# Kernel tuning notes

Hardware: AMD Instinct MI355X
Metric: run time of the kernel (lower is better)

Reference implementation:

```python
import jax, jax.numpy as jnp
import numpy as np

B, S, D, H = 4, 2048, 1024, 16
HD = D // H
SCALE = D ** (-0.5)  # NOTE: original scales by embedding_dim**-0.5, not head_size**-0.5


def setup_inputs() -> dict:
    key = jax.random.key(0)
    k1, k2, k3, k4, k5 = jax.random.split(key, 5)
    return {
        "x": jax.random.normal(k1, (B, S, D), dtype=jnp.float32),
        "Wqkv": jax.random.normal(k2, (3 * D, D), dtype=jnp.float32) * (D ** -0.5),
        "bqkv": jax.random.normal(k3, (3 * D,), dtype=jnp.float32) * 0.02,
        "Wlift": jax.random.normal(k4, (D, D), dtype=jnp.float32) * (D ** -0.5),
        "blift": jax.random.normal(k5, (D,), dtype=jnp.float32) * 0.02,
    }


def reference(x, Wqkv, bqkv, Wlift, blift):
    b, s, d = x.shape
    # qkv projection -> (b, s, 3, H, HD) -> (3, b, H, s, HD)
    qkv = (x @ Wqkv.T + bqkv).reshape(b, s, 3, H, HD).transpose(2, 0, 3, 1, 4)
    q, k, v = qkv[0], qkv[1], qkv[2]  # each (b, H, s, HD)
    # full score matrix, softmax over keys
    scores = jnp.einsum("bhqd,bhkd->bhqk", q, k) * SCALE
    a = jax.nn.softmax(scores, axis=-1)
    # post-hoc causal mask + renormalize (as in the original)
    a = jnp.tril(a)
    a = a / jnp.sum(a, axis=-1, keepdims=True)
    attn = jnp.einsum("bhqk,bhkd->bhqd", a, v)  # (b, H, s, HD)
    attn = attn.swapaxes(1, 2).reshape(b, s, d)  # (b, s, d)
    # lifting linear; Dropout(0.2) is identity in eval mode
    return attn @ Wlift.T + blift
```

## Files before the change

### kernel.cpp

```cpp
#include <hip/hip_runtime.h>
#include <cstdint>
#include <cstddef>

typedef unsigned short u16;
typedef unsigned int u32;
typedef __bf16 bf16x8 __attribute__((ext_vector_type(8)));
typedef float f32x4 __attribute__((ext_vector_type(4)));
typedef float f32x16 __attribute__((ext_vector_type(16)));

__device__ __forceinline__ u16 f2bf(float f) {
  unsigned u = __builtin_bit_cast(unsigned, f);
  return (u16)((u + 0x7FFFu + ((u >> 16) & 1u)) >> 16);
}

__device__ __forceinline__ u32 pk2bf(float lo, float hi) {
  union { __bf16 h[2]; u32 u; } t;
  t.h[0] = (__bf16)lo; t.h[1] = (__bf16)hi;
  return t.u;
}

__device__ __forceinline__ void gl_lds16(const void* g, void* l) {
  __builtin_amdgcn_global_load_lds(
      (const __attribute__((address_space(1))) unsigned int*)g,
      (__attribute__((address_space(3))) unsigned int*)l,
      16, 0, 0);
}

__global__ void cast_all_kernel(const float* __restrict__ x, u16* __restrict__ xo,
                                const float* __restrict__ wq, u16* __restrict__ wqo,
                                const float* __restrict__ wl, u16* __restrict__ wlo) {
  int i = blockIdx.x * blockDim.x + threadIdx.x;
  const float* src;
  u16* dst;
  int k;
  if (i < 2097152) { src = x; dst = xo; k = i; }
  else if (i < 2883584) { src = wq; dst = wqo; k = i - 2097152; }
  else { src = wl; dst = wlo; k = i - 2883584; }
  float4 v = reinterpret_cast<const float4*>(src)[k];
  ushort4 o;
  o.x = f2bf(v.x); o.y = f2bf(v.y); o.z = f2bf(v.z); o.w = f2bf(v.w);
  reinterpret_cast<ushort4*>(dst)[k] = o;
}

template <int EPI>
__global__ __launch_bounds__(256)
void gemm_bt_kernel(const u16* __restrict__ A, const u16* __restrict__ Bw,
                    const float* __restrict__ bias,
                    u16* __restrict__ oq, u16* __restrict__ ok, u16* __restrict__ ovT,
                    float* __restrict__ ofp, int M, int N, int K) {
  __shared__ __align__(16) u16 Als[2][128 * 32];
  __shared__ __align__(16) u16 Bls[2][128 * 32];

  const int tid = threadIdx.x;
  const int lane = tid & 63;
  const int w = tid >> 6, wr = w >> 1, wc = w & 1;
  const int lr = lane & 15, lk = lane >> 4;

  const int nbx = N >> 7;
  const int nb = (M >> 7) * nbx;
  const int vb = (blockIdx.x & 7) * (nb >> 3) + (blockIdx.x >> 3);
  const int brow = (vb / nbx) * 128, bcol = (vb % nbx) * 128;

  const int srow = tid >> 2;
  const int scol = (tid & 3) << 3;
  const u16* ga = A + (size_t)(brow + srow) * K + scol;
  const u16* gb = Bw + (size_t)(bcol + srow) * K + scol;

  f32x4 acc[4][4] = {};

  auto stage = [&](int buf, int kt) {
    const u16* a0 = ga + kt * 32;
    const u16* b0 = gb + kt * 32;
    gl_lds16(a0,             &Als[buf][tid * 8]);
    gl_lds16(a0 + 64 * K,    &Als[buf][2048 + tid * 8]);
    gl_lds16(b0,             &Bls[buf][tid * 8]);
    gl_lds16(b0 + 64 * K,    &Bls[buf][2048 + tid * 8]);
  };

  stage(0, 0);
  __syncthreads();

  const int nt = K >> 5;
  int cur = 0;
  for (int t = 0; t < nt; ++t) {
    if (t + 1 < nt) stage(cur ^ 1, t + 1);
    bf16x8 af[4], bfr[4];
#pragma unroll
    for (int m = 0; m < 4; ++m)
      af[m] = *reinterpret_cast<const bf16x8*>(&Als[cur][(wr * 64 + m * 16 + lr) * 32 + lk * 8]);
#pragma unroll
    for (int n = 0; n < 4; ++n)
      bfr[n] = *reinterpret_cast<const bf16x8*>(&Bls[cur][(wc * 64 + n * 16 + lr) * 32 + lk * 8]);
#pragma unroll
    for (int m = 0; m < 4; ++m)
#pragma unroll
      for (int n = 0; n < 4; ++n)
        acc[m][n] = __builtin_amdgcn_mfma_f32_16x16x32_bf16(af[m], bfr[n], acc[m][n], 0, 0, 0);
    __syncthreads();
    cur ^= 1;
  }

  if (EPI == 0) {
    const int three = bcol >> 10;
#pragma unroll
    for (int n = 0; n < 4; ++n) {
      const int c = bcol + wc * 64 + n * 16 + lr;
      const float bv = bias[c];
      const int cc = c & 1023, h = cc >> 6, hd = cc & 63;
#pragma unroll
      for (int m = 0; m < 4; ++m) {
        const int r0 = brow + wr * 64 + m * 16 + lk * 4;
        const int b = r0 >> 11;
        const int s0 = r0 & 2047;
        if (three == 2) {
          ushort4 pkv;
          pkv.x = f2bf(acc[m][n][0] + bv);
          pkv.y = f2bf(acc[m][n][1] + bv);
          pkv.z = f2bf(acc[m][n][2] + bv);
          pkv.w = f2bf(acc[m][n][3] + bv);
          *reinterpret_cast<ushort4*>(&ovT[((size_t)(b * 16 + h) * 64 + hd) * 2048 + s0]) = pkv;
        } else {
          u16* dst = (three == 0) ? oq : ok;
          const float sc = (three == 0) ? 0.03125f * 1.44269504089f : 1.0f;
#pragma unroll
          for (int j = 0; j < 4; ++j)
            dst[((size_t)(b * 16 + h) * 2048 + (s0 + j)) * 64 + hd] = f2bf((acc[m][n][j] + bv) * sc);
        }
      }
    }
  } else {
#pragma unroll
    for (int n = 0; n < 4; ++n) {
      const int c = bcol + wc * 64 + n * 16 + lr;
      const float bv = bias[c];
#pragma unroll
      for (int m = 0; m < 4; ++m) {
        const int r0 = brow + wr * 64 + m * 16 + lk * 4;
#pragma unroll
        for (int j = 0; j < 4; ++j)
          ofp[(size_t)(r0 + j) * N + c] = acc[m][n][j] + bv;
      }
    }
  }
}

__global__ __launch_bounds__(256, 3)
void attn_causal_kernel(const u16* __restrict__ qg, const u16* __restrict__ kg_,
                        const u16* __restrict__ vT, u16* __restrict__ ob) {
  __shared__ __align__(16) u16 Kls[3][64 * 64];
  __shared__ __align__(16) u16 Vls[3][64 * 64];

  const int tid = threadIdx.x, lane = tid & 63, w = tid >> 6;
  const int n = lane & 31, hi = lane >> 5;
  const int bid = blockIdx.x;
  const int qbi = 15 - (bid >> 6);
  const int bh = bid & 63;
  const int q0w = qbi * 128 + w * 32;
  const int jdiag = qbi * 4 + w;
  const size_t base = (size_t)bh * 2048 * 64;
  const size_t vbase = (size_t)bh * 64 * 2048;

  bf16x8 qf[4];
#pragma unroll
  for (int dc = 0; dc < 4; ++dc)
    qf[dc] = *reinterpret_cast<const bf16x8*>(
        &qg[base + (size_t)(q0w + n) * 64 + dc * 16 + hi * 8]);

  f32x16 o0 = {}, o1 = {};
  float l = 0.f;

  const int ktiles = qbi * 2 + 2;

  const int krow = tid >> 3, kch = tid & 7;

  auto stage = [&](int buf, int t) {
    const int k0 = t << 6;
#pragma unroll
    for (int p = 0; p < 2; ++p) {
      const int r = p * 32 + krow;
      const int sz = (r ^ (r >> 3)) & 7;
      gl_lds16(kg_ + base + (size_t)(k0 + r) * 64 + (kch ^ sz) * 8,
               &Kls[buf][p * 2048 + tid * 8]);
      gl_lds16(vT + vbase + (size_t)r * 2048 + k0 + (kch ^ sz) * 8,
               &Vls[buf][p * 2048 + tid * 8]);
    }
  };

  const int sw0 = ((n ^ (n >> 3)) & 7) << 4;
  const int sw1 = (((32 + n) ^ ((32 + n) >> 3)) & 7) << 4;

  stage(0, 0);
  stage(1, ktiles > 1 ? 1 : 0);
  asm volatile("s_waitcnt vmcnt(4)" ::: "memory");
  __builtin_amdgcn_sched_barrier(0);
  __builtin_amdgcn_s_barrier();
  __builtin_amdgcn_sched_barrier(0);

  bf16x8 pbP0 = {}, pbP1 = {}, vfP00 = {}, vfP01 = {}, vfP10 = {}, vfP11 = {};
  bool pend = false;

  union U { u32 u[4]; bf16x8 v; };

  auto slab = [&](const char* Kb, const char* Vb, int mt, bool diag) {
    const int swK = mt ? sw1 : sw0;
    f32x16 st = {};
    __builtin_amdgcn_s_setprio(1);
#pragma unroll
    for (int dc = 0; dc < 4; ++dc) {
      bf16x8 kf = *reinterpret_cast<const bf16x8*>(
          Kb + (mt * 32 + n) * 128 + ((((dc << 1) | hi) << 4) ^ swK));
      st = __builtin_amdgcn_mfma_f32_32x32x16_bf16(kf, qf[dc], st, 0, 0, 0);
    }
    if (pend) {
      o0 = __builtin_amdgcn_mfma_f32_32x32x16_bf16(vfP00, pbP0, o0, 0, 0, 0);
      o1 = __builtin_amdgcn_mfma_f32_32x32x16_bf16(vfP01, pbP0, o1, 0, 0, 0);
      o0 = __builtin_amdgcn_mfma_f32_32x32x16_bf16(vfP10, pbP1, o0, 0, 0, 0);
      o1 = __builtin_amdgcn_mfma_f32_32x32x16_bf16(vfP11, pbP1, o1, 0, 0, 0);
    }
    __builtin_amdgcn_s_setprio(0);
    if (diag) {
#pragma unroll
      for (int r = 0; r < 16; ++r) {
        const int koff = (r & 3) + 8 * (r >> 2) + 4 * hi;
        if (koff > n) st[r] = -1e30f;
      }
    }
    float rs = 0.f;
#pragma unroll
    for (int r = 0; r < 16; ++r) { st[r] = __builtin_amdgcn_exp2f(st[r]); rs += st[r]; }
    l += rs;
#pragma unroll
    for (int kk = 0; kk < 2; ++kk) {
      const int gown = (kk * 2 + hi) * 4, gsnd = (kk * 2 + (hi ^ 1)) * 4;
      u32 pa0 = pk2bf(st[gown + 0], st[gown + 1]);
      u32 pa1 = pk2bf(st[gown + 2], st[gown + 3]);
      u32 ps0 = pk2bf(st[gsnd + 0], st[gsnd + 1]);
      u32 ps1 = pk2bf(st[gsnd + 2], st[gsnd + 3]);
      u32 rA = __shfl_xor(ps0, 32, 64);
      u32 rB = __shfl_xor(ps1, 32, 64);
      U pb;
      pb.u[0] = hi ? rA : pa0;
      pb.u[1] = hi ? rB : pa1;
      pb.u[2] = hi ? pa0 : rA;
      pb.u[3] = hi ? pa1 : rB;
      if (kk == 0) pbP0 = pb.v; else pbP1 = pb.v;
    }
    const int c0 = ((mt * 4 + hi) << 4);
    const int c1 = ((mt * 4 + 2 + hi) << 4);
    vfP00 = *reinterpret_cast<const bf16x8*>(Vb + n * 128 + (c0 ^ sw0));
    vfP01 = *reinterpret_cast<const bf16x8*>(Vb + (32 + n) * 128 + (c0 ^ sw1));
    vfP10 = *reinterpret_cast<const bf16x8*>(Vb + n * 128 + (c1 ^ sw0));
    vfP11 = *reinterpret_cast<const bf16x8*>(Vb + (32 + n) * 128 + (c1 ^ sw1));
    pend = true;
  };

  for (int t = 0; t < ktiles; ++t) {
    const int tpre = (t + 2 < ktiles) ? (t + 2) : (ktiles - 1);
    stage((t + 2) % 3, tpre);
    const char* Kb = (const char*)&Kls[t % 3][0];
    const char* Vb = (const char*)&Vls[t % 3][0];
    const int e0 = 2 * t;
    if (e0 <= jdiag) slab(Kb, Vb, 0, e0 == jdiag);
    if (e0 + 1 <= jdiag) slab(Kb, Vb, 1, e0 + 1 == jdiag);
    asm volatile("s_waitcnt vmcnt(4)" ::: "memory");
    __builtin_amdgcn_sched_barrier(0);
    __builtin_amdgcn_s_barrier();
    __builtin_amdgcn_sched_barrier(0);
  }

  if (pend) {
    __builtin_amdgcn_s_setprio(1);
    o0 = __builtin_amdgcn_mfma_f32_32x32x16_bf16(vfP00, pbP0, o0, 0, 0, 0);
    o1 = __builtin_amdgcn_mfma_f32_32x32x16_bf16(vfP01, pbP0, o1, 0, 0, 0);
    o0 = __builtin_amdgcn_mfma_f32_32x32x16_bf16(vfP10, pbP1, o0, 0, 0, 0);
    o1 = __builtin_amdgcn_mfma_f32_32x32x16_bf16(vfP11, pbP1, o1, 0, 0, 0);
    __builtin_amdgcn_s_setprio(0);
  }

  asm volatile("s_waitcnt vmcnt(0)" ::: "memory");

  const int b = bh >> 4, h = bh & 15;
  const float lt = l + __shfl_xor(l, 32, 64);
  const float inv = 1.f / lt;
  const size_t rbase = ((size_t)(b * 2048 + q0w + n)) * 1024 + h * 64;
#pragma unroll
  for (int g = 0; g < 4; ++g) {
    ushort4 w0, w1;
    w0.x = f2bf(o0[g * 4 + 0] * inv); w0.y = f2bf(o0[g * 4 + 1] * inv);
    w0.z = f2bf(o0[g * 4 + 2] * inv); w0.w = f2bf(o0[g * 4 + 3] * inv);
    w1.x = f2bf(o1[g * 4 + 0] * inv); w1.y = f2bf(o1[g * 4 + 1] * inv);
    w1.z = f2bf(o1[g * 4 + 2] * inv); w1.w = f2bf(o1[g * 4 + 3] * inv);
    *reinterpret_cast<ushort4*>(&ob[rbase + g * 8 + hi * 4]) = w0;
    *reinterpret_cast<ushort4*>(&ob[rbase + 32 + g * 8 + hi * 4]) = w1;
  }
}

extern "C" void kernel_launch(void* const* d_in, const int* in_sizes, int n_in,
                              void* d_out, int out_size, void* d_ws, size_t ws_size,
                              hipStream_t stream) {
  const float* x     = (const float*)d_in[0];
  const float* Wqkv  = (const float*)d_in[1];
  const float* bqkv  = (const float*)d_in[2];
  const float* Wlift = (const float*)d_in[3];
  const float* blift = (const float*)d_in[4];
  float* out = (float*)d_out;

  if (ws_size < 40ull * 1024 * 1024) return;

  char* ws = (char*)d_ws;
  u16* xb     = (u16*)(ws);
  u16* wqkvb  = (u16*)(ws + 16777216);
  u16* wliftb = (u16*)(ws + 23068672);
  u16* vT     = (u16*)(ws + 25165824);
  u16* attnb  = xb;
  u16* qb = (u16*)d_out;
  u16* kb = qb + 8388608;

  cast_all_kernel<<<12288, 256, 0, stream>>>(x, xb, Wqkv, wqkvb, Wlift, wliftb);

  gemm_bt_kernel<0><<<1536, 256, 0, stream>>>(
      xb, wqkvb, bqkv, qb, kb, vT, nullptr, 8192, 3072, 1024);

  attn_causal_kernel<<<1024, 256, 0, stream>>>(qb, kb, vT, attnb);

  gemm_bt_kernel<1><<<512, 256, 0, stream>>>(
      attnb, wliftb, blift, nullptr, nullptr, nullptr, out, 8192, 1024, 1024);
}
```

Measured before the change: 259.7 us.

## Add dedicated 256x256-tile QKV GEMM with swizzled LDS and wider K step

```diff
diff --git a/kernel.cpp b/kernel.cpp
--- a/kernel.cpp
+++ b/kernel.cpp
@@ -42,12 +42,136 @@
   reinterpret_cast<ushort4*>(dst)[k] = o;
 }
 
-template <int EPI>
+__global__ __launch_bounds__(512, 2)
+void gemm256_qkv_kernel(const u16* __restrict__ A, const u16* __restrict__ Bw,
+                        const float* __restrict__ bias,
+                        u16* __restrict__ oq, u16* __restrict__ ok,
+                        u16* __restrict__ ovT) {
+  __shared__ __align__(16) u16 Als[2][256 * 64];
+  __shared__ __align__(16) u16 Bls[2][256 * 64];
+
+  const int tid = threadIdx.x, lane = tid & 63;
+  const int w = tid >> 6, wr = w >> 2, wc = w & 3;
+  const int lr = lane & 15, lk = lane >> 4;
+
+  const int local = blockIdx.x >> 3, x = blockIdx.x & 7;
+  const int bcol = (local >> 2) * 256;
+  const int brow = (x * 4 + (local & 3)) * 256;
+
+  const u16* ga[4];
+  const u16* gb[4];
+  int dsl[4];
+#pragma unroll
+  for (int p = 0; p < 4; ++p) {
+    const int s = tid + p * 512;
+    const int row = s >> 3, ch = s & 7;
+    const int sc = ch ^ (row & 7);
+    ga[p] = A + (size_t)(brow + row) * 1024 + sc * 8;
+    gb[p] = Bw + (size_t)(bcol + row) * 1024 + sc * 8;
+    dsl[p] = s * 8;
+  }
+
+  auto stage = [&](int buf, int kt) {
+#pragma unroll
+    for (int p = 0; p < 4; ++p) {
+      gl_lds16(ga[p] + kt * 64, &Als[buf][dsl[p]]);
+      gl_lds16(gb[p] + kt * 64, &Bls[buf][dsl[p]]);
+    }
+  };
+
+  f32x4 acc[2][2][4][2] = {};
+
+  stage(0, 0);
+  asm volatile("s_waitcnt vmcnt(0)" ::: "memory");
+  __builtin_amdgcn_s_barrier();
+  __builtin_amdgcn_sched_barrier(0);
+
+  for (int t = 0; t < 16; ++t) {
+    const int buf = t & 1;
+    const char* Ab = (const char*)&Als[buf][0];
+    const char* Bb = (const char*)&Bls[buf][0];
+    if (t + 1 < 16) stage(buf ^ 1, t + 1);
+#pragma unroll
+    for (int mq = 0; mq < 2; ++mq)
+#pragma unroll
+      for (int nq = 0; nq < 2; ++nq) {
+        bf16x8 af[4][2], bfr[2][2];
+#pragma unroll
+        for (int m = 0; m < 4; ++m) {
+          const int ar = wr * 128 + mq * 64 + m * 16 + lr;
+          const int asw = (ar & 7) << 4;
+#pragma unroll
+          for (int ks = 0; ks < 2; ++ks)
+            af[m][ks] = *reinterpret_cast<const bf16x8*>(
+                Ab + ar * 128 + ((ks * 64 + lk * 16) ^ asw));
+        }
+#pragma unroll
+        for (int n = 0; n < 2; ++n) {
+          const int br = wc * 64 + nq * 32 + n * 16 + lr;
+          const int bsw = (br & 7) << 4;
+#pragma unroll
+          for (int ks = 0; ks < 2; ++ks)
+            bfr[n][ks] = *reinterpret_cast<const bf16x8*>(
+                Bb + br * 128 + ((ks * 64 + lk * 16) ^ bsw));
+        }
+        asm volatile("s_waitcnt lgkmcnt(0)" ::: "memory");
+        __builtin_amdgcn_sched_barrier(0);
+        __builtin_amdgcn_s_setprio(1);
+#pragma unroll
+        for (int ks = 0; ks < 2; ++ks)
+#pragma unroll
+          for (int m = 0; m < 4; ++m)
+#pragma unroll
+            for (int n = 0; n < 2; ++n)
+              acc[mq][nq][m][n] = __builtin_amdgcn_mfma_f32_16x16x32_bf16(
+                  af[m][ks], bfr[n][ks], acc[mq][nq][m][n], 0, 0, 0);
+        __builtin_amdgcn_s_setprio(0);
+      }
+    asm volatile("s_waitcnt vmcnt(0)" ::: "memory");
+    __builtin_amdgcn_s_barrier();
+    __builtin_amdgcn_sched_barrier(0);
+  }
+
+  const int three = bcol >> 10;
+#pragma unroll
+  for (int mq = 0; mq < 2; ++mq)
+#pragma unroll
+    for (int nq = 0; nq < 2; ++nq)
+#pragma unroll
+      for (int n = 0; n < 2; ++n) {
+        const int c = bcol + wc * 64 + nq * 32 + n * 16 + lr;
+        const float bv = bias[c];
+        const int cc = c & 1023, h = cc >> 6, hd = cc & 63;
+#pragma unroll
+        for (int m = 0; m < 4; ++m) {
+          const int r0 = brow + wr * 128 + mq * 64 + m * 16 + lk * 4;
+          const int b = r0 >> 11;
+          const int s0 = r0 & 2047;
+          const f32x4& a4 = acc[mq][nq][m][n];
+          if (three == 2) {
+            ushort4 pkv;
+            pkv.x = f2bf(a4[0] + bv);
+            pkv.y = f2bf(a4[1] + bv);
+            pkv.z = f2bf(a4[2] + bv);
+            pkv.w = f2bf(a4[3] + bv);
+            *reinterpret_cast<ushort4*>(
+                &ovT[((size_t)(b * 16 + h) * 64 + hd) * 2048 + s0]) = pkv;
+          } else {
+            u16* dst = (three == 0) ? oq : ok;
+            const float sc = (three == 0) ? 0.03125f * 1.44269504089f : 1.0f;
+#pragma unroll
+            for (int j = 0; j < 4; ++j)
+              dst[((size_t)(b * 16 + h) * 2048 + (s0 + j)) * 64 + hd] =
+                  f2bf((a4[j] + bv) * sc);
+          }
+        }
+      }
+}
+
 __global__ __launch_bounds__(256)
-void gemm_bt_kernel(const u16* __restrict__ A, const u16* __restrict__ Bw,
-                    const float* __restrict__ bias,
-                    u16* __restrict__ oq, u16* __restrict__ ok, u16* __restrict__ ovT,
-                    float* __restrict__ ofp, int M, int N, int K) {
+void gemm_lift_kernel(const u16* __restrict__ A, const u16* __restrict__ Bw,
+                      const float* __restrict__ bias, float* __restrict__ ofp,
+                      int M, int N, int K) {
   __shared__ __align__(16) u16 Als[2][128 * 32];
   __shared__ __align__(16) u16 Bls[2][128 * 32];
 
@@ -100,46 +224,16 @@
     cur ^= 1;
   }
 
-  if (EPI == 0) {
-    const int three = bcol >> 10;
-#pragma unroll
-    for (int n = 0; n < 4; ++n) {
-      const int c = bcol + wc * 64 + n * 16 + lr;
-      const float bv = bias[c];
-      const int cc = c & 1023, h = cc >> 6, hd = cc & 63;
-#pragma unroll
-      for (int m = 0; m < 4; ++m) {
-        const int r0 = brow + wr * 64 + m * 16 + lk * 4;
-        const int b = r0 >> 11;
-        const int s0 = r0 & 2047;
-        if (three == 2) {
-          ushort4 pkv;
-          pkv.x = f2bf(acc[m][n][0] + bv);
-          pkv.y = f2bf(acc[m][n][1] + bv);
-          pkv.z = f2bf(acc[m][n][2] + bv);
-          pkv.w = f2bf(acc[m][n][3] + bv);
-          *reinterpret_cast<ushort4*>(&ovT[((size_t)(b * 16 + h) * 64 + hd) * 2048 + s0]) = pkv;
-        } else {
-          u16* dst = (three == 0) ? oq : ok;
-          const float sc = (three == 0) ? 0.03125f * 1.44269504089f : 1.0f;
-#pragma unroll
-          for (int j = 0; j < 4; ++j)
-            dst[((size_t)(b * 16 + h) * 2048 + (s0 + j)) * 64 + hd] = f2bf((acc[m][n][j] + bv) * sc);
-        }
-      }
-    }
-  } else {
-#pragma unroll
-    for (int n = 0; n < 4; ++n) {
-      const int c = bcol + wc * 64 + n * 16 + lr;
-      const float bv = bias[c];
-#pragma unroll
-      for (int m = 0; m < 4; ++m) {
-        const int r0 = brow + wr * 64 + m * 16 + lk * 4;
-#pragma unroll
-        for (int j = 0; j < 4; ++j)
-          ofp[(size_t)(r0 + j) * N + c] = acc[m][n][j] + bv;
-      }
+#pragma unroll
+  for (int n = 0; n < 4; ++n) {
+    const int c = bcol + wc * 64 + n * 16 + lr;
+    const float bv = bias[c];
+#pragma unroll
+    for (int m = 0; m < 4; ++m) {
+      const int r0 = brow + wr * 64 + m * 16 + lk * 4;
+#pragma unroll
+      for (int j = 0; j < 4; ++j)
+        ofp[(size_t)(r0 + j) * N + c] = acc[m][n][j] + bv;
     }
   }
 }
@@ -318,11 +412,10 @@
 
   cast_all_kernel<<<12288, 256, 0, stream>>>(x, xb, Wqkv, wqkvb, Wlift, wliftb);
 
-  gemm_bt_kernel<0><<<1536, 256, 0, stream>>>(
-      xb, wqkvb, bqkv, qb, kb, vT, nullptr, 8192, 3072, 1024);
+  gemm256_qkv_kernel<<<384, 512, 0, stream>>>(xb, wqkvb, bqkv, qb, kb, vT);
 
   attn_causal_kernel<<<1024, 256, 0, stream>>>(qb, kb, vT, attnb);
 
-  gemm_bt_kernel<1><<<512, 256, 0, stream>>>(
-      attnb, wliftb, blift, nullptr, nullptr, nullptr, out, 8192, 1024, 1024);
-}
+  gemm_lift_kernel<<<512, 256, 0, stream>>>(
+      attnb, wliftb, blift, out, 8192, 1024, 1024);
+}
```

Measured after the change: 273.7 us. 5.4% more time.

## Split causal attention KV range across two blocks with atomic fp32 combine

Applied to the files above, without the earlier changes.

```diff
diff --git a/kernel.cpp b/kernel.cpp
--- a/kernel.cpp
+++ b/kernel.cpp
@@ -144,19 +144,24 @@
   }
 }
 
-__global__ __launch_bounds__(256, 3)
-void attn_causal_kernel(const u16* __restrict__ qg, const u16* __restrict__ kg_,
-                        const u16* __restrict__ vT, u16* __restrict__ ob) {
-  __shared__ __align__(16) u16 Kls[3][64 * 64];
-  __shared__ __align__(16) u16 Vls[3][64 * 64];
+__global__ __launch_bounds__(256, 5)
+void attn_split_kernel(const u16* __restrict__ qg, const u16* __restrict__ kg_,
+                       const u16* __restrict__ vT, float* __restrict__ Of,
+                       float* __restrict__ lf) {
+  __shared__ __align__(16) u16 Kls[2][64 * 64];
+  __shared__ __align__(16) u16 Vls[2][64 * 64];
 
   const int tid = threadIdx.x, lane = tid & 63, w = tid >> 6;
   const int n = lane & 31, hi = lane >> 5;
   const int bid = blockIdx.x;
-  const int qbi = 15 - (bid >> 6);
-  const int bh = bid & 63;
+  const int half = bid & 1;
+  const int rest = bid >> 1;
+  const int qbi = 15 - (rest >> 6);
+  const int bh = rest & 63;
   const int q0w = qbi * 128 + w * 32;
   const int jdiag = qbi * 4 + w;
+  const int t0 = half ? (qbi + 1) : 0;
+  const int ntiles = qbi + 1;
   const size_t base = (size_t)bh * 2048 * 64;
   const size_t vbase = (size_t)bh * 64 * 2048;
 
@@ -168,8 +173,6 @@
 
   f32x16 o0 = {}, o1 = {};
   float l = 0.f;
-
-  const int ktiles = qbi * 2 + 2;
 
   const int krow = tid >> 3, kch = tid & 7;
 
@@ -189,12 +192,8 @@
   const int sw0 = ((n ^ (n >> 3)) & 7) << 4;
   const int sw1 = (((32 + n) ^ ((32 + n) >> 3)) & 7) << 4;
 
-  stage(0, 0);
-  stage(1, ktiles > 1 ? 1 : 0);
-  asm volatile("s_waitcnt vmcnt(4)" ::: "memory");
-  __builtin_amdgcn_sched_barrier(0);
-  __builtin_amdgcn_s_barrier();
-  __builtin_amdgcn_sched_barrier(0);
+  stage(0, t0);
+  __syncthreads();
 
   bf16x8 pbP0 = {}, pbP1 = {}, vfP00 = {}, vfP01 = {}, vfP10 = {}, vfP11 = {};
   bool pend = false;
@@ -254,6 +253,163 @@
     pend = true;
   };
 
+  for (int tt = 0; tt < ntiles; ++tt) {
+    const int t = t0 + tt;
+    if (tt + 1 < ntiles) stage((tt + 1) & 1, t + 1);
+    const char* Kb = (const char*)&Kls[tt & 1][0];
+    const char* Vb = (const char*)&Vls[tt & 1][0];
+    const int e0 = 2 * t;
+    if (e0 <= jdiag) slab(Kb, Vb, 0, e0 == jdiag);
+    if (e0 + 1 <= jdiag) slab(Kb, Vb, 1, e0 + 1 == jdiag);
+    __syncthreads();
+  }
+
+  if (pend) {
+    __builtin_amdgcn_s_setprio(1);
+    o0 = __builtin_amdgcn_mfma_f32_32x32x16_bf16(vfP00, pbP0, o0, 0, 0, 0);
+    o1 = __builtin_amdgcn_mfma_f32_32x32x16_bf16(vfP01, pbP0, o1, 0, 0, 0);
+    o0 = __builtin_amdgcn_mfma_f32_32x32x16_bf16(vfP10, pbP1, o0, 0, 0, 0);
+    o1 = __builtin_amdgcn_mfma_f32_32x32x16_bf16(vfP11, pbP1, o1, 0, 0, 0);
+    __builtin_amdgcn_s_setprio(0);
+  }
+
+  const float lt = l + __shfl_xor(l, 32, 64);
+  const size_t qrow = (size_t)bh * 2048 + q0w + n;
+  if (hi == 0) atomicAdd(&lf[qrow], lt);
+  float* Orow = Of + qrow * 64;
+#pragma unroll
+  for (int r = 0; r < 16; ++r) {
+    const int d = (r & 3) + 8 * (r >> 2) + 4 * hi;
+    atomicAdd(&Orow[d], o0[r]);
+    atomicAdd(&Orow[32 + d], o1[r]);
+  }
+}
+
+__global__ __launch_bounds__(256)
+void combine_kernel(const float* __restrict__ Of, const float* __restrict__ lf,
+                    u16* __restrict__ ob) {
+  const int tid = blockIdx.x * 256 + threadIdx.x;
+  const int row = tid >> 4;
+  const int d4 = (tid & 15) * 4;
+  const int bh = row >> 11, q = row & 2047;
+  const int b = bh >> 4, h = bh & 15;
+  const float inv = 1.f / lf[row];
+  const float4 v = *reinterpret_cast<const float4*>(Of + (size_t)row * 64 + d4);
+  ushort4 o;
+  o.x = f2bf(v.x * inv); o.y = f2bf(v.y * inv);
+  o.z = f2bf(v.z * inv); o.w = f2bf(v.w * inv);
+  *reinterpret_cast<ushort4*>(&ob[((size_t)(b * 2048 + q)) * 1024 + h * 64 + d4]) = o;
+}
+
+__global__ __launch_bounds__(256, 3)
+void attn_causal_kernel(const u16* __restrict__ qg, const u16* __restrict__ kg_,
+                        const u16* __restrict__ vT, u16* __restrict__ ob) {
+  __shared__ __align__(16) u16 Kls[3][64 * 64];
+  __shared__ __align__(16) u16 Vls[3][64 * 64];
+
+  const int tid = threadIdx.x, lane = tid & 63, w = tid >> 6;
+  const int n = lane & 31, hi = lane >> 5;
+  const int bid = blockIdx.x;
+  const int qbi = 15 - (bid >> 6);
+  const int bh = bid & 63;
+  const int q0w = qbi * 128 + w * 32;
+  const int jdiag = qbi * 4 + w;
+  const size_t base = (size_t)bh * 2048 * 64;
+  const size_t vbase = (size_t)bh * 64 * 2048;
+
+  bf16x8 qf[4];
+#pragma unroll
+  for (int dc = 0; dc < 4; ++dc)
+    qf[dc] = *reinterpret_cast<const bf16x8*>(
+        &qg[base + (size_t)(q0w + n) * 64 + dc * 16 + hi * 8]);
+
+  f32x16 o0 = {}, o1 = {};
+  float l = 0.f;
+
+  const int ktiles = qbi * 2 + 2;
+  const int krow = tid >> 3, kch = tid & 7;
+
+  auto stage = [&](int buf, int t) {
+    const int k0 = t << 6;
+#pragma unroll
+    for (int p = 0; p < 2; ++p) {
+      const int r = p * 32 + krow;
+      const int sz = (r ^ (r >> 3)) & 7;
+      gl_lds16(kg_ + base + (size_t)(k0 + r) * 64 + (kch ^ sz) * 8,
+               &Kls[buf][p * 2048 + tid * 8]);
+      gl_lds16(vT + vbase + (size_t)r * 2048 + k0 + (kch ^ sz) * 8,
+               &Vls[buf][p * 2048 + tid * 8]);
+    }
+  };
+
+  const int sw0 = ((n ^ (n >> 3)) & 7) << 4;
+  const int sw1 = (((32 + n) ^ ((32 + n) >> 3)) & 7) << 4;
+
+  stage(0, 0);
+  stage(1, ktiles > 1 ? 1 : 0);
+  asm volatile("s_waitcnt vmcnt(4)" ::: "memory");
+  __builtin_amdgcn_sched_barrier(0);
+  __builtin_amdgcn_s_barrier();
+  __builtin_amdgcn_sched_barrier(0);
+
+  bf16x8 pbP0 = {}, pbP1 = {}, vfP00 = {}, vfP01 = {}, vfP10 = {}, vfP11 = {};
+  bool pend = false;
+
+  union U { u32 u[4]; bf16x8 v; };
+
+  auto slab = [&](const char* Kb, const char* Vb, int mt, bool diag) {
+    const int swK = mt ? sw1 : sw0;
+    f32x16 st = {};
+    __builtin_amdgcn_s_setprio(1);
+#pragma unroll
+    for (int dc = 0; dc < 4; ++dc) {
+      bf16x8 kf = *reinterpret_cast<const bf16x8*>(
+          Kb + (mt * 32 + n) * 128 + ((((dc << 1) | hi) << 4) ^ swK));
+      st = __builtin_amdgcn_mfma_f32_32x32x16_bf16(kf, qf[dc], st, 0, 0, 0);
+    }
+    if (pend) {
+      o0 = __builtin_amdgcn_mfma_f32_32x32x16_bf16(vfP00, pbP0, o0, 0, 0, 0);
+      o1 = __builtin_amdgcn_mfma_f32_32x32x16_bf16(vfP01, pbP0, o1, 0, 0, 0);
+      o0 = __builtin_amdgcn_mfma_f32_32x32x16_bf16(vfP10, pbP1, o0, 0, 0, 0);
+      o1 = __builtin_amdgcn_mfma_f32_32x32x16_bf16(vfP11, pbP1, o1, 0, 0, 0);
+    }
+    __builtin_amdgcn_s_setprio(0);
+    if (diag) {
+#pragma unroll
+      for (int r = 0; r < 16; ++r) {
+        const int koff = (r & 3) + 8 * (r >> 2) + 4 * hi;
+        if (koff > n) st[r] = -1e30f;
+      }
+    }
+    float rs = 0.f;
+#pragma unroll
+    for (int r = 0; r < 16; ++r) { st[r] = __builtin_amdgcn_exp2f(st[r]); rs += st[r]; }
+    l += rs;
+#pragma unroll
+    for (int kk = 0; kk < 2; ++kk) {
+      const int gown = (kk * 2 + hi) * 4, gsnd = (kk * 2 + (hi ^ 1)) * 4;
+      u32 pa0 = pk2bf(st[gown + 0], st[gown + 1]);
+      u32 pa1 = pk2bf(st[gown + 2], st[gown + 3]);
+      u32 ps0 = pk2bf(st[gsnd + 0], st[gsnd + 1]);
+      u32 ps1 = pk2bf(st[gsnd + 2], st[gsnd + 3]);
+      u32 rA = __shfl_xor(ps0, 32, 64);
+      u32 rB = __shfl_xor(ps1, 32, 64);
+      U pb;
+      pb.u[0] = hi ? rA : pa0;
+      pb.u[1] = hi ? rB : pa1;
+      pb.u[2] = hi ? pa0 : rA;
+      pb.u[3] = hi ? pa1 : rB;
+      if (kk == 0) pbP0 = pb.v; else pbP1 = pb.v;
+    }
+    const int c0 = ((mt * 4 + hi) << 4);
+    const int c1 = ((mt * 4 + 2 + hi) << 4);
+    vfP00 = *reinterpret_cast<const bf16x8*>(Vb + n * 128 + (c0 ^ sw0));
+    vfP01 = *reinterpret_cast<const bf16x8*>(Vb + (32 + n) * 128 + (c0 ^ sw1));
+    vfP10 = *reinterpret_cast<const bf16x8*>(Vb + n * 128 + (c1 ^ sw0));
+    vfP11 = *reinterpret_cast<const bf16x8*>(Vb + (32 + n) * 128 + (c1 ^ sw1));
+    pend = true;
+  };
+
   for (int t = 0; t < ktiles; ++t) {
     const int tpre = (t + 2 < ktiles) ? (t + 2) : (ktiles - 1);
     stage((t + 2) % 3, tpre);
@@ -316,12 +472,22 @@
   u16* qb = (u16*)d_out;
   u16* kb = qb + 8388608;
 
+  const bool split = ws_size >= 76021760ull;
+  float* Of = (float*)(ws + 41943040);
+  float* lf = (float*)(ws + 75497472);
+
   cast_all_kernel<<<12288, 256, 0, stream>>>(x, xb, Wqkv, wqkvb, Wlift, wliftb);
 
   gemm_bt_kernel<0><<<1536, 256, 0, stream>>>(
       xb, wqkvb, bqkv, qb, kb, vT, nullptr, 8192, 3072, 1024);
 
-  attn_causal_kernel<<<1024, 256, 0, stream>>>(qb, kb, vT, attnb);
+  if (split) {
+    hipMemsetAsync(ws + 41943040, 0, 34078720, stream);
+    attn_split_kernel<<<2048, 256, 0, stream>>>(qb, kb, vT, Of, lf);
+    combine_kernel<<<8192, 256, 0, stream>>>(Of, lf, attnb);
+  } else {
+    attn_causal_kernel<<<1024, 256, 0, stream>>>(qb, kb, vT, attnb);
+  }
 
   gemm_bt_kernel<1><<<512, 256, 0, stream>>>(
       attnb, wliftb, blift, nullptr, nullptr, nullptr, out, 8192, 1024, 1024);
```

Result: slower. 711.9 us (+174.1%).
